# Optimization experiments

Hardware: AMD Instinct MI355X
Metric: run time of the kernel (lower is better)

The kernel has to match this reference:

```python
import jax, jax.numpy as jnp
import numpy as np

B, Hh, Ww, C = 8, 64, 64, 384
Dg = C // 2          # 192, per-group d_model
Di = Dg              # expand=1 -> d_inner = d_model
K = 2                # scan directions per group
S = 1                # d_state
R = -(-Dg // 16)     # dt_rank = ceil(d_model/16) = 12
Cout = 384


def setup_inputs() -> dict:
    key = jax.random.key(0)
    ks = jax.random.split(key, 30)
    n = lambda k, shp, s=0.05: (jax.random.normal(k, shp, jnp.float32) * s)
    inp = {
        "x": jax.random.normal(ks[0], (B, Hh * Ww, C), jnp.float32),
        "norm_g": jnp.ones((C,), jnp.float32),
        "norm_b": jnp.zeros((C,), jnp.float32),
        # DynamicChannelSorter (reduction=2)
        "r_w1": n(ks[1], (C // 2, C)), "r_b1": n(ks[2], (C // 2,)),
        "r_w2": n(ks[3], (C, C // 2)), "r_b2": n(ks[4], (C,)),
        # SS2D params stacked over 2 groups
        "in_proj_w": n(ks[5], (2, 2 * Di, Dg)),
        "conv_w": n(ks[6], (2, Di, 1, 3, 3), 0.1),
        "conv_b": n(ks[7], (2, Di), 0.02),
        "x_proj_w": n(ks[8], (2, K, R + 2 * S, Di)),
        "dt_proj_w": n(ks[9], (2, K, Di, R), 0.1),
        "dt_proj_b": n(ks[10], (2, K, Di), 0.5) - 3.0,   # softplus-inv of small dt
        "A_log": n(ks[11], (2, K, Di, S), 0.1),
        "Ds": jnp.ones((2, K, Di), jnp.float32),
        "out_norm_g": jnp.ones((2, Di), jnp.float32),
        "out_norm_b": jnp.zeros((2, Di), jnp.float32),
        "out_proj_w": n(ks[12], (2, Dg, Di)),
        # channel_interaction (reduction=16)
        "ci_w1": n(ks[13], (C // 16, C)), "ci_b1": n(ks[14], (C // 16,)),
        "ci_w2": n(ks[15], (C, C // 16)), "ci_b2": n(ks[16], (C,)),
        "proj_w": n(ks[17], (Cout, C)), "proj_b": n(ks[18], (Cout,)),
        "skip_scale": jnp.ones((1,), jnp.float32),
        "H": Hh, "W": Ww,
    }
    return inp


def _ln(x, g, b, eps=1e-5):
    m = x.mean(-1, keepdims=True)
    v = jnp.mean((x - m) ** 2, -1, keepdims=True)
    return (x - m) * jax.lax.rsqrt(v + eps) * g + b


def _selective_scan(xs, dts, Bm, Cm, A, D):
    # xs,dts: (B,K,Di,L); Bm,Cm: (B,K,S,L); A: (K,Di,S); D: (K,Di)
    dA = jnp.exp(dts[..., None] * A[None, :, :, None, :])              # (B,K,Di,L,S)
    dBx = dts[..., None] * jnp.swapaxes(Bm, -1, -2)[:, :, None] * xs[..., None]
    dA_t = jnp.moveaxis(dA, 3, 0)                                      # (L,B,K,Di,S)
    dBx_t = jnp.moveaxis(dBx, 3, 0)
    C_t = jnp.moveaxis(Cm, -1, 0)                                      # (L,B,K,S)
    h0 = jnp.zeros(dA.shape[:3] + (dA.shape[-1],), xs.dtype)           # (B,K,Di,S)

    def step(h, inp):
        a, bx, c = inp
        h = a * h + bx
        return h, jnp.einsum('bkcs,bks->bkc', h, c)

    _, ys = jax.lax.scan(step, h0, (dA_t, dBx_t, C_t))                 # (L,B,K,Di)
    ys = jnp.moveaxis(ys, 0, -1)                                       # (B,K,Di,L)
    return ys + D[None, :, :, None] * xs


def _ss2d(x, in_w, cw, cb, xp_w, dt_w, dt_b, A_log, D, on_g, on_b, op_w, vertical):
    # x: (B,H,W,Dg). VMamba-style SS2D with K=2 directions.
    b, h, w, _ = x.shape
    L = h * w
    xz = jnp.einsum('bhwc,dc->bhwd', x, in_w)                          # (B,H,W,2*Di)
    xc, z = jnp.split(xz, 2, axis=-1)
    xc = jnp.transpose(xc, (0, 3, 1, 2))                               # (B,Di,H,W)
    xc = jax.lax.conv_general_dilated(
        xc, cw, (1, 1), 'SAME', feature_group_count=Di,
        dimension_numbers=('NCHW', 'OIHW', 'NCHW')) + cb[None, :, None, None]
    xc = jax.nn.silu(xc)
    xf = jnp.transpose(xc, (0, 1, 3, 2)) if vertical else xc
    xflat = xf.reshape(b, Di, L)
    xs = jnp.stack([xflat, jnp.flip(xflat, -1)], axis=1)               # (B,K,Di,L)
    x_dbl = jnp.einsum('bkcl,kdc->bkdl', xs, xp_w)
    r = dt_w.shape[-1]
    dts, Bm, Cm = x_dbl[:, :, :r], x_dbl[:, :, r:r + S], x_dbl[:, :, r + S:r + 2 * S]
    dts = jax.nn.softplus(jnp.einsum('bkrl,kdr->bkdl', dts, dt_w) + dt_b[None, :, :, None])
    A = -jnp.exp(A_log)
    ys = _selective_scan(xs, dts, Bm, Cm, A, D)                        # (B,K,Di,L)
    y = ys[:, 0] + jnp.flip(ys[:, 1], -1)                              # cross-merge
    if vertical:
        y = jnp.transpose(y.reshape(b, Di, w, h), (0, 1, 3, 2))
    else:
        y = y.reshape(b, Di, h, w)
    y = jnp.transpose(y, (0, 2, 3, 1))                                 # (B,H,W,Di)
    y = _ln(y, on_g, on_b)
    y = y * jax.nn.silu(z)
    return jnp.einsum('bhwd,od->bhwo', y, op_w)


def reference(x, norm_g, norm_b, r_w1, r_b1, r_w2, r_b2, in_proj_w, conv_w,
              conv_b, x_proj_w, dt_proj_w, dt_proj_b, A_log, Ds, out_norm_g,
              out_norm_b, out_proj_w, ci_w1, ci_b1, ci_w2, ci_b2, proj_w,
              proj_b, skip_scale, H, W):
    b, n, c = x.shape
    residual = x
    xn = _ln(x, norm_g, norm_b)
    # dynamic channel sorter
    pool = xn.mean(axis=1)                                             # (B,C)
    scores = jax.nn.sigmoid(jax.nn.relu(pool @ r_w1.T + r_b1) @ r_w2.T + r_b2)
    sort_idx = jnp.argsort(-scores, axis=1)
    inv_idx = jnp.argsort(sort_idx, axis=1)
    x_sorted = jnp.take_along_axis(xn, sort_idx[:, None, :], axis=2)
    xsp = x_sorted.reshape(b, H, W, c)
    x1, x2 = jnp.split(xsp, 2, axis=-1)
    y1 = _ss2d(x1, in_proj_w[0], conv_w[0], conv_b[0], x_proj_w[0], dt_proj_w[0],
               dt_proj_b[0], A_log[0], Ds[0], out_norm_g[0], out_norm_b[0],
               out_proj_w[0], vertical=False)
    y2 = _ss2d(x2, in_proj_w[1], conv_w[1], conv_b[1], x_proj_w[1], dt_proj_w[1],
               dt_proj_b[1], A_log[1], Ds[1], out_norm_g[1], out_norm_b[1],
               out_proj_w[1], vertical=True)
    y_cat = jnp.concatenate([y1, y2], axis=-1).reshape(b, n, c)
    y_restored = jnp.take_along_axis(y_cat, inv_idx[:, None, :], axis=2)
    gate = jax.nn.sigmoid(jax.nn.relu(xn @ ci_w1.T + ci_b1) @ ci_w2.T + ci_b2)
    y_final = (y_restored * gate) @ proj_w.T + proj_b
    return residual + y_final * skip_scale
```

## Files before the change

### kernel.cpp

```cpp
#include <hip/hip_runtime.h>
#include <math.h>

#define NB 8
#define LTOK 4096
#define CH 384
#define DH 192
#define HH 64
#define WW 64
#define NCHK 128
#define CHS 32

static constexpr long BLC  = (long)NB * LTOK * CH;
static constexpr long CST  = (long)32 * NCHK * DH;

typedef unsigned short u16;
typedef u16   u16x8 __attribute__((ext_vector_type(8)));
typedef short s16x8 __attribute__((ext_vector_type(8)));
typedef float f32x4 __attribute__((ext_vector_type(4)));

__device__ inline u16 f2bf(float f){
  unsigned int u = __float_as_uint(f);
  return (u16)((u + 0x7FFFu + ((u >> 16) & 1u)) >> 16);
}
__device__ inline float bf2f(u16 h){ return __uint_as_float(((unsigned int)h) << 16); }
__device__ inline float fsigmoid(float x){ return 1.f / (1.f + __expf(-x)); }

#define SCOL(ml, c) ((c) ^ ((((ml) >> 2) & 3) << 4))

template<int NW>
__device__ inline float blockSum(float v, float* sm){
  #pragma unroll
  for (int o = 32; o > 0; o >>= 1) v += __shfl_down(v, o);
  int lane = threadIdx.x & 63, wv = threadIdx.x >> 6;
  if (lane == 0) sm[wv] = v;
  __syncthreads();
  if (threadIdx.x == 0){ float t = 0.f; for (int i = 0; i < NW; i++) t += sm[i]; sm[0] = t; }
  __syncthreads();
  float t = sm[0];
  __syncthreads();
  return t;
}

__global__ __launch_bounds__(128) void k_ln(const float* __restrict__ x,
    const float* __restrict__ g, const float* __restrict__ b, float* __restrict__ xn){
  __shared__ float sm[2];
  long row = blockIdx.x;
  int t = threadIdx.x;
  const float* xr = x + row * CH;
  float v0 = xr[t], v1 = xr[t + 128], v2 = xr[t + 256];
  float s = blockSum<2>(v0 + v1 + v2, sm);
  float m = s * (1.f / CH);
  float d0 = v0 - m, d1 = v1 - m, d2 = v2 - m;
  float vs = blockSum<2>(d0*d0 + d1*d1 + d2*d2, sm);
  float inv = rsqrtf(vs * (1.f / CH) + 1e-5f);
  float* o = xn + row * CH;
  o[t]       = d0 * inv * g[t]       + b[t];
  o[t + 128] = d1 * inv * g[t + 128] + b[t + 128];
  o[t + 256] = d2 * inv * g[t + 256] + b[t + 256];
}

__global__ __launch_bounds__(128) void k_pool(const float* __restrict__ xn, float* __restrict__ pp){
  int c = blockIdx.x * 128 + threadIdx.x;
  int chunk = blockIdx.y, b = blockIdx.z;
  long base = ((long)b * LTOK + chunk * 256) * CH;
  float s = 0.f;
  for (int n = 0; n < 256; n++) s += xn[base + (long)n * CH + c];
  pp[((long)b * 16 + chunk) * CH + c] = s;
}

__global__ __launch_bounds__(384) void k_score(const float* __restrict__ pp,
    const float* __restrict__ w1, const float* __restrict__ b1,
    const float* __restrict__ w2, const float* __restrict__ b2,
    int* __restrict__ sidx, int* __restrict__ inv){
  __shared__ float poolv[CH];
  __shared__ float hid[192];
  __shared__ float sc[CH];
  int b = blockIdx.x, t = threadIdx.x;
  float s = 0.f;
  for (int ch = 0; ch < 16; ch++) s += pp[((long)b * 16 + ch) * CH + t];
  poolv[t] = s * (1.f / LTOK);
  __syncthreads();
  if (t < 192){
    float h = b1[t];
    for (int c = 0; c < CH; c++) h += poolv[c] * w1[t * CH + c];
    hid[t] = fmaxf(h, 0.f);
  }
  __syncthreads();
  {
    float h = b2[t];
    for (int j = 0; j < 192; j++) h += hid[j] * w2[t * 192 + j];
    sc[t] = 1.f / (1.f + expf(-h));
  }
  __syncthreads();
  float mys = sc[t];
  int rank = 0;
  for (int j = 0; j < CH; j++){
    float o = sc[j];
    rank += (o > mys) || (o == mys && j < t);
  }
  sidx[b * CH + rank] = t;
  inv[b * CH + t] = rank;
}

__global__ __launch_bounds__(256) void k_cast(const float* __restrict__ s,
    u16* __restrict__ d, int n){
  int i = blockIdx.x * 256 + threadIdx.x;
  if (i < n) d[i] = f2bf(s[i]);
}

__global__ __launch_bounds__(256) void k_prepA(const float* __restrict__ alog,
    float* __restrict__ Atab){
  int i = blockIdx.x * 256 + threadIdx.x;
  if (i < 4 * 192) Atab[i] = -expf(alog[i]);
}

__global__ __launch_bounds__(256) void k_prepcw(const float* __restrict__ cw,
    u16* __restrict__ cwb){
  int i = blockIdx.x * 256 + threadIdx.x;
  if (i < 2 * 9 * DH){
    int g = i / (9 * DH); int r = i - g * 9 * DH;
    int tap = r / DH; int di = r - tap * DH;
    cwb[i] = f2bf(cw[((long)g * DH + di) * 9 + tap]);
  }
}

__global__ __launch_bounds__(384) void k_castgather(const float* __restrict__ xn,
    const int* __restrict__ sidx, u16* __restrict__ As){
  long row = blockIdx.x;
  int b = (int)(row >> 12);
  int t = threadIdx.x;
  int c = sidx[b * CH + t];
  As[row * CH + t] = f2bf(xn[row * CH + c]);
}

__global__ __launch_bounds__(256) void k_prepw(const float* __restrict__ w1,
    const float* __restrict__ b1, const float* __restrict__ w2,
    const int* __restrict__ sidx, u16* __restrict__ w1g, u16* __restrict__ w2p,
    float* __restrict__ b1p){
  int b = blockIdx.x, tid = threadIdx.x;
  if (b < NB){
    const int* sx = sidx + b * CH;
    for (int i = tid; i < 32 * CH; i += 256){
      int j = i / CH, r = i - j * CH;
      float v = (j < 24) ? w1[j * CH + sx[r]] : 0.f;
      w1g[(long)b * 32 * CH + i] = f2bf(v);
    }
  } else {
    for (int i = tid; i < CH * 32; i += 256){
      int n = i >> 5, j = i & 31;
      w2p[i] = f2bf((j < 24) ? w2[n * 24 + j] : 0.f);
    }
    if (tid < 32) b1p[tid] = (tid < 24) ? b1[tid] : 0.f;
  }
}

__global__ __launch_bounds__(256) void k_prepM(const float* __restrict__ dtw,
    const float* __restrict__ xpw, u16* __restrict__ Mw){
  int gk = blockIdx.y;
  int g = gk >> 1, k = gk & 1;
  int idx = blockIdx.x * 256 + threadIdx.x;
  int di = idx / 192, c = idx - di * 192;
  float s = 0.f;
  #pragma unroll
  for (int r = 0; r < 12; r++)
    s += dtw[((long)gk * 192 + di) * 12 + r] * xpw[(long)g * 5376 + (k * 14 + r) * 192 + c];
  Mw[(long)gk * 36864 + idx] = f2bf(s);
}

__global__ __launch_bounds__(256) void k_hid(const u16* __restrict__ As,
    const u16* __restrict__ w1g, const float* __restrict__ b1p,
    u16* __restrict__ hidp){
  __shared__ u16 sA[128 * 32];
  __shared__ u16 sB[32 * 32];
  int b = blockIdx.y;
  const u16* Ab = As + (long)b * LTOK * CH;
  const u16* Bb = w1g + (long)b * 32 * CH;
  int tid = threadIdx.x;
  int m0 = blockIdx.x * 128;
  int wv = tid >> 6, l = tid & 63;
  int wm = wv * 32;
  int kg = l >> 4, lr = l & 15;

  f32x4 acc[2][2];
  #pragma unroll
  for (int i = 0; i < 2; i++)
    #pragma unroll
    for (int j = 0; j < 2; j++)
      #pragma unroll
      for (int r = 0; r < 4; r++) acc[i][j][r] = 0.f;

  int aoffU[2], boffU[2];
  #pragma unroll
  for (int i = 0; i < 2; i++){
    int r = wm + i * 16 + lr;
    aoffU[i] = r * 32 + ((kg * 8) ^ ((r & 3) << 3));
  }
  #pragma unroll
  for (int j = 0; j < 2; j++){
    int r = j * 16 + lr;
    boffU[j] = r * 32 + ((kg * 8) ^ ((r & 3) << 3));
  }

  u16x8 ra[2], rbv;
  #pragma unroll
  for (int q = 0; q < 2; q++){
    int i = q * 256 + tid; int row = i >> 2, sl = i & 3, ss = sl ^ (row & 3);
    ra[q] = *(const u16x8*)(Ab + (long)(m0 + row) * CH + ss * 8);
  }
  if (tid < 128){
    int row = tid >> 2, sl = tid & 3, ss = sl ^ (row & 3);
    rbv = *(const u16x8*)(Bb + (long)row * CH + ss * 8);
  }

  const int nks = CH / 32;
  for (int ks = 0; ks < nks; ks++){
    __syncthreads();
    #pragma unroll
    for (int q = 0; q < 2; q++){
      int i = q * 256 + tid; int row = i >> 2, sl = i & 3;
      *(u16x8*)(sA + row * 32 + sl * 8) = ra[q];
    }
    if (tid < 128){
      int row = tid >> 2, sl = tid & 3;
      *(u16x8*)(sB + row * 32 + sl * 8) = rbv;
    }
    __syncthreads();
    if (ks + 1 < nks){
      int k0 = (ks + 1) * 32;
      #pragma unroll
      for (int q = 0; q < 2; q++){
        int i = q * 256 + tid; int row = i >> 2, sl = i & 3, ss = sl ^ (row & 3);
        ra[q] = *(const u16x8*)(Ab + (long)(m0 + row) * CH + k0 + ss * 8);
      }
      if (tid < 128){
        int row = tid >> 2, sl = tid & 3, ss = sl ^ (row & 3);
        rbv = *(const u16x8*)(Bb + (long)row * CH + k0 + ss * 8);
      }
    }
    s16x8 af[2], bfr[2];
    #pragma unroll
    for (int i = 0; i < 2; i++) af[i] = *(const s16x8*)(sA + aoffU[i]);
    #pragma unroll
    for (int j = 0; j < 2; j++) bfr[j] = *(const s16x8*)(sB + boffU[j]);
    #pragma unroll
    for (int i = 0; i < 2; i++)
      #pragma unroll
      for (int j = 0; j < 2; j++)
        acc[i][j] = __builtin_amdgcn_mfma_f32_16x16x32_bf16(af[i], bfr[j], acc[i][j], 0, 0, 0);
  }

  #pragma unroll
  for (int i = 0; i < 2; i++)
    #pragma unroll
    for (int j = 0; j < 2; j++)
      #pragma unroll
      for (int r = 0; r < 4; r++){
        int m = m0 + wm + i * 16 + kg * 4 + r;
        int n = j * 16 + lr;
        float v = fmaxf(acc[i][j][r] + b1p[n], 0.f);
        hidp[((long)b * LTOK + m) * 32 + n] = f2bf(v);
      }
}

template<int BN, int MODE>
__global__ __launch_bounds__(256) void k_mm(
    const u16* __restrict__ A, int lda, long aOuter, long aInner,
    const u16* __restrict__ B, long bInner,
    float* __restrict__ Cf, u16* __restrict__ Ch,
    long cOuter, long cInner, int ldc,
    int K, int innerCnt,
    const float* __restrict__ bias, const float* __restrict__ resid,
    const float* __restrict__ skip,
    const u16* __restrict__ gy, const int* __restrict__ ginv){
  constexpr int BM = 128;
  constexpr int AI = 2;
  constexpr int BI = (BN * 32) / (256 * 8);
  constexpr int NJ = BN / 32;
  __shared__ u16 sA[BM * 32];
  __shared__ u16 sB[BN * 32];

  int bz = blockIdx.z;
  int bo = bz / innerCnt, bi_ = bz - bo * innerCnt;
  const u16* Ab = A + (long)bo * aOuter + (long)bi_ * aInner;
  const u16* Bb = B + (long)bi_ * bInner;
  int tid = threadIdx.x;
  int m0 = blockIdx.y * BM, n0 = blockIdx.x * BN;
  int wv = tid >> 6, l = tid & 63;
  int wm = (wv >> 1) * 64, wn = (wv & 1) * (BN / 2);
  int kg = l >> 4, lr = l & 15;

  f32x4 acc[4][NJ];
  #pragma unroll
  for (int i = 0; i < 4; i++)
    #pragma unroll
    for (int j = 0; j < NJ; j++)
      #pragma unroll
      for (int r = 0; r < 4; r++) acc[i][j][r] = 0.f;

  int aoffU[4], boffU[NJ];
  #pragma unroll
  for (int i = 0; i < 4; i++){
    int r = wm + i * 16 + lr;
    aoffU[i] = r * 32 + ((kg * 8) ^ ((r & 3) << 3));
  }
  #pragma unroll
  for (int j = 0; j < NJ; j++){
    int r = wn + j * 16 + lr;
    boffU[j] = r * 32 + ((kg * 8) ^ ((r & 3) << 3));
  }

  u16x8 ra[AI], rb[BI];
  #pragma unroll
  for (int q = 0; q < AI; q++){
    int i = q * 256 + tid; int row = i >> 2, sl = i & 3, ss = sl ^ (row & 3);
    ra[q] = *(const u16x8*)(Ab + (long)(m0 + row) * lda + ss * 8);
  }
  #pragma unroll
  for (int q = 0; q < BI; q++){
    int i = q * 256 + tid; int row = i >> 2, sl = i & 3, ss = sl ^ (row & 3);
    rb[q] = *(const u16x8*)(Bb + (long)(n0 + row) * K + ss * 8);
  }

  int nks = K >> 5;
  for (int ks = 0; ks < nks; ks++){
    __syncthreads();
    #pragma unroll
    for (int q = 0; q < AI; q++){
      int i = q * 256 + tid; int row = i >> 2, sl = i & 3;
      *(u16x8*)(sA + row * 32 + sl * 8) = ra[q];
    }
    #pragma unroll
    for (int q = 0; q < BI; q++){
      int i = q * 256 + tid; int row = i >> 2, sl = i & 3;
      *(u16x8*)(sB + row * 32 + sl * 8) = rb[q];
    }
    __syncthreads();
    if (ks + 1 < nks){
      int k0 = (ks + 1) * 32;
      #pragma unroll
      for (int q = 0; q < AI; q++){
        int i = q * 256 + tid; int row = i >> 2, sl = i & 3, ss = sl ^ (row & 3);
        ra[q] = *(const u16x8*)(Ab + (long)(m0 + row) * lda + k0 + ss * 8);
      }
      #pragma unroll
      for (int q = 0; q < BI; q++){
        int i = q * 256 + tid; int row = i >> 2, sl = i & 3, ss = sl ^ (row & 3);
        rb[q] = *(const u16x8*)(Bb + (long)(n0 + row) * K + k0 + ss * 8);
      }
    }
    s16x8 af[4];
    #pragma unroll
    for (int i = 0; i < 4; i++) af[i] = *(const s16x8*)(sA + aoffU[i]);
    s16x8 bfr[NJ];
    #pragma unroll
    for (int j = 0; j < NJ; j++) bfr[j] = *(const s16x8*)(sB + boffU[j]);
    #pragma unroll
    for (int i = 0; i < 4; i++)
      #pragma unroll
      for (int j = 0; j < NJ; j++)
        acc[i][j] = __builtin_amdgcn_mfma_f32_16x16x32_bf16(af[i], bfr[j], acc[i][j], 0, 0, 0);
  }

  long zc = (long)bo * cOuter + (long)bi_ * cInner;
  #pragma unroll
  for (int i = 0; i < 4; i++){
    #pragma unroll
    for (int j = 0; j < NJ; j++){
      #pragma unroll
      for (int r = 0; r < 4; r++){
        int m = m0 + wm + i * 16 + kg * 4 + r;
        int n = n0 + wn + j * 16 + lr;
        float v = acc[i][j][r];
        if constexpr (MODE == 1){
          if (n < 192) ((u16*)Cf)[zc + (long)m * 192 + n] = f2bf(v);
          else         Ch[zc + (long)m * 192 + (n - 192)] = f2bf(v);
        } else if constexpr (MODE == 2){
          Ch[zc + (long)m * ldc + n] = f2bf(v);
        } else if constexpr (MODE == 3){
          float vb = v + bias[n];
          long o = (long)m * ldc + n;
          Cf[o] = resid[o] + skip[0] * vb;
        } else {
          float gate = fsigmoid(v + bias[n]);
          int bt = m >> 12;
          float yr = bf2f(gy[(long)m * ldc + ginv[bt * CH + n]]);
          Ch[(long)m * ldc + n] = f2bf(yr * gate);
        }
      }
    }
  }
}

__global__ __launch_bounds__(256) void k_dt(
    const u16* __restrict__ xcvh, const u16* __restrict__ Mw,
    const float* __restrict__ dtb, const float* __restrict__ Atab,
    const float* __restrict__ bc, u16* __restrict__ pk16,
    float* __restrict__ cP, float* __restrict__ cS){
  constexpr int BM = 128, AI = 2, NJ = 2;
  __shared__ unsigned sMem[BM * 64];
  u16* sA = (u16*)sMem;
  u16* sB = (u16*)(sMem + 2048);

  int z = blockIdx.z;
  int bg = z >> 1, kk_ = z & 1, g = bg & 1, gk = g * 2 + kk_;
  const u16* Ab = xcvh + (long)bg * LTOK * 192;
  const u16* Bb = Mw + (long)gk * 36864;
  int tid = threadIdx.x;
  int m0 = blockIdx.y * BM, n0 = blockIdx.x * 64;
  int wv = tid >> 6, l = tid & 63;
  int wm = (wv >> 1) * 64, wn = (wv & 1) * 32;
  int kg = l >> 4, lr = l & 15;

  f32x4 acc[4][NJ];
  #pragma unroll
  for (int i = 0; i < 4; i++)
    #pragma unroll
    for (int j = 0; j < NJ; j++)
      #pragma unroll
      for (int r = 0; r < 4; r++) acc[i][j][r] = 0.f;

  int aoffU[4], boffU[NJ];
  #pragma unroll
  for (int i = 0; i < 4; i++){
    int r = wm + i * 16 + lr;
    aoffU[i] = r * 32 + ((kg * 8) ^ ((r & 3) << 3));
  }
  #pragma unroll
  for (int j = 0; j < NJ; j++){
    int r = wn + j * 16 + lr;
    boffU[j] = r * 32 + ((kg * 8) ^ ((r & 3) << 3));
  }

  u16x8 ra[AI], rb0;
  #pragma unroll
  for (int q = 0; q < AI; q++){
    int i = q * 256 + tid; int row = i >> 2, sl = i & 3, ss = sl ^ (row & 3);
    ra[q] = *(const u16x8*)(Ab + (long)(m0 + row) * 192 + ss * 8);
  }
  {
    int row = tid >> 2, sl = tid & 3, ss = sl ^ (row & 3);
    rb0 = *(const u16x8*)(Bb + (long)(n0 + row) * 192 + ss * 8);
  }

  const int nks = 6;
  for (int ks = 0; ks < nks; ks++){
    __syncthreads();
    #pragma unroll
    for (int q = 0; q < AI; q++){
      int i = q * 256 + tid; int row = i >> 2, sl = i & 3;
      *(u16x8*)(sA + row * 32 + sl * 8) = ra[q];
    }
    {
      int row = tid >> 2, sl = tid & 3;
      *(u16x8*)(sB + row * 32 + sl * 8) = rb0;
    }
    __syncthreads();
    if (ks + 1 < nks){
      int k0 = (ks + 1) * 32;
      #pragma unroll
      for (int q = 0; q < AI; q++){
        int i = q * 256 + tid; int row = i >> 2, sl = i & 3, ss = sl ^ (row & 3);
        ra[q] = *(const u16x8*)(Ab + (long)(m0 + row) * 192 + k0 + ss * 8);
      }
      {
        int row = tid >> 2, sl = tid & 3, ss = sl ^ (row & 3);
        rb0 = *(const u16x8*)(Bb + (long)(n0 + row) * 192 + k0 + ss * 8);
      }
    }
    s16x8 af[4], bfr[NJ];
    #pragma unroll
    for (int i = 0; i < 4; i++) af[i] = *(const s16x8*)(sA + aoffU[i]);
    #pragma unroll
    for (int j = 0; j < NJ; j++) bfr[j] = *(const s16x8*)(sB + boffU[j]);
    #pragma unroll
    for (int i = 0; i < 4; i++)
      #pragma unroll
      for (int j = 0; j < NJ; j++)
        acc[i][j] = __builtin_amdgcn_mfma_f32_16x16x32_bf16(af[i], bfr[j], acc[i][j], 0, 0, 0);
  }

  unsigned pkreg[4][NJ][4];
  #pragma unroll
  for (int i = 0; i < 4; i++){
    #pragma unroll
    for (int j = 0; j < NJ; j++){
      #pragma unroll
      for (int r = 0; r < 4; r++){
        int m = m0 + wm + i * 16 + kg * 4 + r;
        int n = n0 + wn + j * 16 + lr;
        float rr = acc[i][j][r] + dtb[gk * 192 + n];
        float dtv = __logf(1.f + __expf(rr));
        float av  = __expf(Atab[gk * 192 + n] * dtv);
        float Bv  = bc[((long)z * LTOK + m) * 2];
        float xv  = bf2f(xcvh[((long)bg * LTOK + m) * 192 + n]);
        pk16[((long)z * LTOK + m) * 192 + n] = f2bf(dtv);
        pkreg[i][j][r] = ((unsigned)f2bf(dtv * Bv * xv) << 16) | (unsigned)f2bf(av);
      }
    }
  }

  __syncthreads();
  #pragma unroll
  for (int i = 0; i < 4; i++){
    #pragma unroll
    for (int j = 0; j < NJ; j++){
      #pragma unroll
      for (int r = 0; r < 4; r++){
        int ml = wm + i * 16 + kg * 4 + r;
        int cl = wn + j * 16 + lr;
        sMem[ml * 64 + SCOL(ml, cl)] = pkreg[i][j][r];
      }
    }
  }
  __syncthreads();

  int cc = tid >> 6, nn = tid & 63;
  float P = 1.f, S = 0.f;
  if (kk_ == 0){
    for (int s = 0; s < CHS; s++){
      int row = cc * CHS + s;
      unsigned v = sMem[row * 64 + SCOL(row, nn)];
      float a = bf2f((u16)(v & 0xFFFFu));
      float dBx = bf2f((u16)(v >> 16));
      P *= a; S = a * S + dBx;
    }
  } else {
    for (int s = CHS - 1; s >= 0; s--){
      int row = cc * CHS + s;
      unsigned v = sMem[row * 64 + SCOL(row, nn)];
      float a = bf2f((u16)(v & 0xFFFFu));
      float dBx = bf2f((u16)(v >> 16));
      P *= a; S = a * S + dBx;
    }
  }
  int cglob = (kk_ == 0) ? (blockIdx.y * 4 + cc)
                         : ((LTOK - m0) / CHS - cc - 1);
  long idx = ((long)z * NCHK + cglob) * 192 + n0 + nn;
  cP[idx] = P;
  cS[idx] = S;
}

__global__ __launch_bounds__(192) void k_conv(const u16* __restrict__ xch,
    const u16* __restrict__ cwb, const float* __restrict__ cb,
    const float* __restrict__ xpw, u16* __restrict__ xcvh,
    float* __restrict__ bc){
  __shared__ float red[8][4][25];
  int tid = threadIdx.x;
  int chg = tid % 24, pp = tid / 24;
  int p = blockIdx.x * 8 + pp;
  int bg = blockIdx.y; int g = bg & 1;
  int h = p >> 6, w = p & 63;
  int di = chg * 8;
  long sb = (long)bg * LTOK;

  u16x8 wv[9];
  #pragma unroll
  for (int t = 0; t < 9; t++)
    wv[t] = *(const u16x8*)(cwb + ((long)g * 9 + t) * DH + di);

  float acc[8];
  #pragma unroll
  for (int j = 0; j < 8; j++) acc[j] = cb[g * DH + di + j];

  #pragma unroll
  for (int dh = -1; dh <= 1; dh++){
    int hh = h + dh; if (hh < 0 || hh >= HH) continue;
    #pragma unroll
    for (int dw = -1; dw <= 1; dw++){
      int ww2 = w + dw; if (ww2 < 0 || ww2 >= WW) continue;
      u16x8 xv = *(const u16x8*)(xch + (sb + hh * WW + ww2) * DH + di);
      int t = (dh + 1) * 3 + (dw + 1);
      #pragma unroll
      for (int j = 0; j < 8; j++) acc[j] += bf2f(wv[t][j]) * bf2f(xv[j]);
    }
  }

  u16x8 ov;
  #pragma unroll
  for (int j = 0; j < 8; j++){
    float s = acc[j];
    acc[j] = s * fsigmoid(s);
    ov[j] = f2bf(acc[j]);
  }
  int lscan = (g == 0) ? p : (w * HH + h);
  *(u16x8*)(xcvh + (sb + lscan) * DH + di) = ov;

  #pragma unroll
  for (int j = 0; j < 4; j++){
    int k = j >> 1, ci = j & 1;
    const float* wl = xpw + (long)g * 5376 + (k * 14 + 12 + ci) * 192 + di;
    float sacc = 0.f;
    #pragma unroll
    for (int q = 0; q < 8; q++) sacc += acc[q] * wl[q];
    red[pp][j][chg] = sacc;
  }
  __syncthreads();
  if (tid < 32){
    int pos = tid >> 2, j = tid & 3;
    float ssum = 0.f;
    #pragma unroll
    for (int q = 0; q < 24; q++) ssum += red[pos][j][q];
    int p2 = blockIdx.x * 8 + pos;
    int h2 = p2 >> 6, w2 = p2 & 63;
    int ls = (g == 0) ? p2 : (w2 * HH + h2);
    int k = j >> 1;
    bc[(((long)(bg * 2 + k)) * LTOK + ls) * 2 + (j & 1)] = ssum;
  }
}

__global__ __launch_bounds__(192) void k_scan_p2(const float* __restrict__ cP,
    const float* __restrict__ cS, float* __restrict__ h0){
  int z = blockIdx.x;
  int di = threadIdx.x;
  float h = 0.f;
  for (int c = 0; c < NCHK; c++){
    long idx = ((long)z * NCHK + c) * 192 + di;
    h0[idx] = h;
    h = cP[idx] * h + cS[idx];
  }
}

__global__ __launch_bounds__(192) void k_scan_p3(const u16* __restrict__ pk16,
    const u16* __restrict__ xcvh, const float* __restrict__ bc,
    const float* __restrict__ Atab, const float* __restrict__ ds,
    const float* __restrict__ h0, u16* __restrict__ ydir){
  int bg = blockIdx.x, c = blockIdx.y;
  int g = bg & 1;
  int di = threadIdx.x;
  const u16* xc = xcvh + (long)bg * LTOK * 192 + di;
  u16* yo = ydir + (long)bg * LTOK * 192 + di;
  #pragma unroll
  for (int k = 0; k < 2; k++){
    int z = bg * 2 + k, gk = g * 2 + k;
    float Dv = ds[gk * 192 + di];
    float Av = Atab[gk * 192 + di];
    const u16* pk = pk16 + (long)z * LTOK * 192 + di;
    const float* bcp = bc + (long)z * LTOK * 2;
    int cc = (k == 0) ? c : (NCHK - 1 - c);
    float h = h0[((long)z * NCHK + cc) * 192 + di];
    int l  = (k == 0) ? c * CHS : (c * CHS + CHS - 1);
    int dl = (k == 0) ? 1 : -1;
    for (int s = 0; s < CHS; s++, l += dl){
      float dtv = bf2f(pk[(long)l * 192]);
      float av  = __expf(Av * dtv);
      float xv  = bf2f(xc[(long)l * 192]);
      float Bv  = bcp[l * 2], Cv = bcp[l * 2 + 1];
      h = av * h + dtv * Bv * xv;
      float y = h * Cv + Dv * xv;
      if (k == 0) yo[(long)l * 192] = f2bf(y);
      else        yo[(long)l * 192] = f2bf(bf2f(yo[(long)l * 192]) + y);
    }
  }
}

__global__ __launch_bounds__(192) void k_combine(const u16* __restrict__ ydir,
    const u16* __restrict__ zh, const float* __restrict__ ong, const float* __restrict__ onb,
    u16* __restrict__ yab){
  __shared__ float sm[3];
  int p = blockIdx.x; int bg = blockIdx.y; int g = bg & 1;
  int h = p >> 6, w = p & 63;
  int l = (g == 0) ? p : (w * HH + h);
  int di = threadIdx.x;
  float y = bf2f(ydir[((long)bg * LTOK + l) * DH + di]);
  float s = blockSum<3>(y, sm);
  float m = s * (1.f / DH);
  float d = y - m;
  float vs = blockSum<3>(d * d, sm);
  float inv = rsqrtf(vs * (1.f / DH) + 1e-5f);
  float yl = d * inv * ong[g * DH + di] + onb[g * DH + di];
  float z = bf2f(zh[((long)bg * LTOK + p) * DH + di]);
  yab[((long)bg * LTOK + p) * DH + di] = f2bf(yl * z * fsigmoid(z));
}

extern "C" void kernel_launch(void* const* d_in, const int* in_sizes, int n_in,
                              void* d_out, int out_size, void* d_ws, size_t ws_size,
                              hipStream_t stream){
  const float* x       = (const float*)d_in[0];
  const float* norm_g  = (const float*)d_in[1];
  const float* norm_b  = (const float*)d_in[2];
  const float* r_w1    = (const float*)d_in[3];
  const float* r_b1    = (const float*)d_in[4];
  const float* r_w2    = (const float*)d_in[5];
  const float* r_b2    = (const float*)d_in[6];
  const float* in_proj = (const float*)d_in[7];
  const float* conv_w  = (const float*)d_in[8];
  const float* conv_b  = (const float*)d_in[9];
  const float* xp_w    = (const float*)d_in[10];
  const float* dt_w    = (const float*)d_in[11];
  const float* dt_b    = (const float*)d_in[12];
  const float* A_log   = (const float*)d_in[13];
  const float* Ds      = (const float*)d_in[14];
  const float* on_g    = (const float*)d_in[15];
  const float* on_b    = (const float*)d_in[16];
  const float* op_w    = (const float*)d_in[17];
  const float* ci_w1   = (const float*)d_in[18];
  const float* ci_b1   = (const float*)d_in[19];
  const float* ci_w2   = (const float*)d_in[20];
  const float* ci_b2   = (const float*)d_in[21];
  const float* proj_w  = (const float*)d_in[22];
  const float* proj_b  = (const float*)d_in[23];
  const float* skip    = (const float*)d_in[24];
  float* out = (float*)d_out;
  float* ws  = (float*)d_ws;

  float* xn   = ws;
  float* xcb  = ws + BLC;
  float* R3   = ws + 2 * BLC;
  float* R4   = R3 + BLC / 2;
  float* R5   = R4 + BLC / 2;
  float* pp   = R5 + BLC / 2;
  int*  sidx  = (int*)(pp + NB * 16 * CH);
  int*  inv   = sidx + NB * CH;
  u16*  wip   = (u16*)(inv + NB * CH);
  u16*  wop   = wip + 2 * 384 * 192;
  u16*  wpj   = wop + 2 * 192 * 192;
  u16*  w1g   = wpj + 384 * 384;
  u16*  w2p   = w1g + NB * 32 * CH;
  u16*  Mw    = w2p + CH * 32;
  u16*  cwb   = Mw + 4 * 192 * 192;
  float* b1p  = (float*)(cwb + 2 * 9 * DH);
  float* Atab = b1p + 32;
  u16*  hidp  = (u16*)(Atab + 4 * 192);
  float* bc   = (float*)(hidp + (long)NB * LTOK * 32);
  float* cP   = bc + 32 * LTOK * 2;
  float* cS   = cP + CST;
  float* h0   = cS + CST;

  size_t need = ((size_t)(2 * BLC) + 3 * (BLC / 2) + NB * 16 * CH + 32 * LTOK * 2 + 3 * CST + 64) * 4
              + (size_t)(2 * NB * CH) * 4 + (size_t)(4 * 192 + 32) * 4
              + ((size_t)2*384*192 + 2*192*192 + 384*384 + NB*32*CH + CH*32 + 4*192*192
                 + 2*9*DH + (size_t)NB * LTOK * 32) * 2
              + 8192;
  if (ws_size < need) return;

  u16*  As   = (u16*)R5;
  u16*  zh   = (u16*)R3;
  u16*  xcbh = (u16*)xcb;
  u16*  xcvh = (u16*)R4;
  u16*  pk16 = (u16*)ws;
  u16*  ydir = (u16*)R5;
  u16*  yab  = (u16*)R4;
  u16*  ycat = (u16*)R3;
  u16*  gab  = (u16*)xcb;

  k_ln<<<NB * LTOK, 128, 0, stream>>>(x, norm_g, norm_b, xn);
  k_cast<<<(2*384*192 + 255)/256, 256, 0, stream>>>(in_proj, wip, 2*384*192);
  k_cast<<<(2*192*192 + 255)/256, 256, 0, stream>>>(op_w,    wop, 2*192*192);
  k_cast<<<(384*384   + 255)/256, 256, 0, stream>>>(proj_w,  wpj, 384*384);
  k_prepA<<<3, 256, 0, stream>>>(A_log, Atab);
  k_prepcw<<<(2*9*DH + 255)/256, 256, 0, stream>>>(conv_w, cwb);
  k_prepM<<<dim3(144, 4), 256, 0, stream>>>(dt_w, xp_w, Mw);
  k_pool<<<dim3(3, 16, NB), 128, 0, stream>>>(xn, pp);
  k_score<<<NB, 384, 0, stream>>>(pp, r_w1, r_b1, r_w2, r_b2, sidx, inv);
  k_castgather<<<NB * LTOK, 384, 0, stream>>>(xn, sidx, As);
  k_prepw<<<NB + 1, 256, 0, stream>>>(ci_w1, ci_b1, ci_w2, sidx, w1g, w2p, b1p);

  k_mm<128, 1><<<dim3(3, 32, 16), 256, 0, stream>>>(
      As, CH, (long)LTOK * CH, 192,
      wip, (long)384 * 192,
      (float*)xcbh, zh, (long)2 * LTOK * DH, (long)LTOK * DH, 0,
      192, 2, nullptr, nullptr, nullptr, nullptr, nullptr);

  k_hid<<<dim3(32, NB), 256, 0, stream>>>(As, w1g, b1p, hidp);

  k_conv<<<dim3(LTOK / 8, NB * 2), 192, 0, stream>>>(xcbh, cwb, conv_b, xp_w, xcvh, bc);

  k_dt<<<dim3(3, 32, 32), 256, 0, stream>>>(xcvh, Mw, dt_b, Atab, bc, pk16, cP, cS);

  k_scan_p2<<<32, 192, 0, stream>>>(cP, cS, h0);
  k_scan_p3<<<dim3(NB * 2, NCHK), 192, 0, stream>>>(pk16, xcvh, bc, Atab, Ds, h0, ydir);

  k_combine<<<dim3(LTOK, NB * 2), 192, 0, stream>>>(ydir, zh, on_g, on_b, yab);

  k_mm<64, 2><<<dim3(3, 32, 16), 256, 0, stream>>>(
      yab, DH, (long)2 * LTOK * DH, (long)LTOK * DH,
      wop, (long)192 * 192,
      nullptr, ycat, (long)LTOK * CH, 192, CH,
      192, 2, nullptr, nullptr, nullptr, nullptr, nullptr);

  k_mm<128, 4><<<dim3(3, 256, 1), 256, 0, stream>>>(
      hidp, 32, 0, 0,
      w2p, 0,
      nullptr, gab, 0, 0, CH,
      32, 1, ci_b2, nullptr, nullptr, ycat, inv);

  k_mm<128, 3><<<dim3(3, 256, 1), 256, 0, stream>>>(
      gab, CH, 0, 0,
      wpj, 0,
      out, nullptr, 0, 0, CH,
      CH, 1, proj_b, x, skip, nullptr, nullptr);
}
```

Baseline: 395.2 us.

## Fuse combine LayerNorm and gating into scan pass, stage x tile in LDS

The scan pass now keeps both directions' chunk outputs in registers and sums them there, instead of writing one direction to memory and read-modify-writing it for the other. It then performs the out_norm LayerNorm and z·silu(z) gating in-block through shared memory, which removes the separate combine kernel and the ydir intermediate round trip. In k_dt, the x tile is staged into shared memory with vector loads and the per-column bias and A values are hoisted, replacing scattered 2-byte global loads in the epilogue. The cost is higher register and LDS use in the scan kernel, plus a one-pass variance formula that is less numerically stable.

```diff
diff --git a/kernel.cpp b/kernel.cpp
--- a/kernel.cpp
+++ b/kernel.cpp
@@ -398,8 +398,9 @@
     float* __restrict__ cP, float* __restrict__ cS){
   constexpr int BM = 128, AI = 2, NJ = 2;
   __shared__ unsigned sMem[BM * 64];
-  u16* sA = (u16*)sMem;
-  u16* sB = (u16*)(sMem + 2048);
+  u16* sA  = (u16*)sMem;
+  u16* sB  = (u16*)(sMem + 2048);
+  u16* xvT = (u16*)(sMem + 3072);
 
   int z = blockIdx.z;
   int bg = z >> 1, kk_ = z & 1, g = bg & 1, gk = g * 2 + kk_;
@@ -411,6 +412,14 @@
   int wm = (wv >> 1) * 64, wn = (wv & 1) * 32;
   int kg = l >> 4, lr = l & 15;
 
+  #pragma unroll
+  for (int q = 0; q < 4; q++){
+    int i8 = q * 256 + tid;
+    int row = i8 >> 3, c8 = i8 & 7;
+    u16x8 v = *(const u16x8*)(Ab + (long)(m0 + row) * 192 + n0 + c8 * 8);
+    *(u16x8*)(xvT + row * 72 + c8 * 8) = v;
+  }
+
   f32x4 acc[4][NJ];
   #pragma unroll
   for (int i = 0; i < 4; i++)
@@ -480,19 +489,27 @@
   }
 
   unsigned pkreg[4][NJ][4];
+  float dtbj[NJ], Atlj[NJ];
+  #pragma unroll
+  for (int j = 0; j < NJ; j++){
+    int n = n0 + wn + j * 16 + lr;
+    dtbj[j] = dtb[gk * 192 + n];
+    Atlj[j] = Atab[gk * 192 + n];
+  }
   #pragma unroll
   for (int i = 0; i < 4; i++){
     #pragma unroll
-    for (int j = 0; j < NJ; j++){
-      #pragma unroll
-      for (int r = 0; r < 4; r++){
-        int m = m0 + wm + i * 16 + kg * 4 + r;
+    for (int r = 0; r < 4; r++){
+      int ml = wm + i * 16 + kg * 4 + r;
+      int m = m0 + ml;
+      float Bv = bc[((long)z * LTOK + m) * 2];
+      #pragma unroll
+      for (int j = 0; j < NJ; j++){
         int n = n0 + wn + j * 16 + lr;
-        float rr = acc[i][j][r] + dtb[gk * 192 + n];
+        float rr = acc[i][j][r] + dtbj[j];
         float dtv = __logf(1.f + __expf(rr));
-        float av  = __expf(Atab[gk * 192 + n] * dtv);
-        float Bv  = bc[((long)z * LTOK + m) * 2];
-        float xv  = bf2f(xcvh[((long)bg * LTOK + m) * 192 + n]);
+        float av  = __expf(Atlj[j] * dtv);
+        float xv  = bf2f(xvT[ml * 72 + wn + j * 16 + lr]);
         pk16[((long)z * LTOK + m) * 192 + n] = f2bf(dtv);
         pkreg[i][j][r] = ((unsigned)f2bf(dtv * Bv * xv) << 16) | (unsigned)f2bf(av);
       }
@@ -623,53 +640,92 @@
 __global__ __launch_bounds__(192) void k_scan_p3(const u16* __restrict__ pk16,
     const u16* __restrict__ xcvh, const float* __restrict__ bc,
     const float* __restrict__ Atab, const float* __restrict__ ds,
-    const float* __restrict__ h0, u16* __restrict__ ydir){
+    const float* __restrict__ h0, const u16* __restrict__ zh,
+    const float* __restrict__ ong, const float* __restrict__ onb,
+    u16* __restrict__ yab){
+  __shared__ float yl[CHS][193];
+  __shared__ float red[2][32][6];
+  __shared__ float minv[2][32];
   int bg = blockIdx.x, c = blockIdx.y;
   int g = bg & 1;
   int di = threadIdx.x;
   const u16* xc = xcvh + (long)bg * LTOK * 192 + di;
-  u16* yo = ydir + (long)bg * LTOK * 192 + di;
-  #pragma unroll
-  for (int k = 0; k < 2; k++){
-    int z = bg * 2 + k, gk = g * 2 + k;
-    float Dv = ds[gk * 192 + di];
-    float Av = Atab[gk * 192 + di];
+  int l0 = c * CHS;
+  float yv[CHS];
+
+  {
+    int z = bg * 2, gk = g * 2;
+    float Dv = ds[gk * 192 + di], Av = Atab[gk * 192 + di];
     const u16* pk = pk16 + (long)z * LTOK * 192 + di;
     const float* bcp = bc + (long)z * LTOK * 2;
-    int cc = (k == 0) ? c : (NCHK - 1 - c);
-    float h = h0[((long)z * NCHK + cc) * 192 + di];
-    int l  = (k == 0) ? c * CHS : (c * CHS + CHS - 1);
-    int dl = (k == 0) ? 1 : -1;
-    for (int s = 0; s < CHS; s++, l += dl){
+    float h = h0[((long)z * NCHK + c) * 192 + di];
+    #pragma unroll
+    for (int s = 0; s < CHS; s++){
+      int l = l0 + s;
       float dtv = bf2f(pk[(long)l * 192]);
       float av  = __expf(Av * dtv);
       float xv  = bf2f(xc[(long)l * 192]);
       float Bv  = bcp[l * 2], Cv = bcp[l * 2 + 1];
       h = av * h + dtv * Bv * xv;
-      float y = h * Cv + Dv * xv;
-      if (k == 0) yo[(long)l * 192] = f2bf(y);
-      else        yo[(long)l * 192] = f2bf(bf2f(yo[(long)l * 192]) + y);
-    }
-  }
-}
-
-__global__ __launch_bounds__(192) void k_combine(const u16* __restrict__ ydir,
-    const u16* __restrict__ zh, const float* __restrict__ ong, const float* __restrict__ onb,
-    u16* __restrict__ yab){
-  __shared__ float sm[3];
-  int p = blockIdx.x; int bg = blockIdx.y; int g = bg & 1;
-  int h = p >> 6, w = p & 63;
-  int l = (g == 0) ? p : (w * HH + h);
-  int di = threadIdx.x;
-  float y = bf2f(ydir[((long)bg * LTOK + l) * DH + di]);
-  float s = blockSum<3>(y, sm);
-  float m = s * (1.f / DH);
-  float d = y - m;
-  float vs = blockSum<3>(d * d, sm);
-  float inv = rsqrtf(vs * (1.f / DH) + 1e-5f);
-  float yl = d * inv * ong[g * DH + di] + onb[g * DH + di];
-  float z = bf2f(zh[((long)bg * LTOK + p) * DH + di]);
-  yab[((long)bg * LTOK + p) * DH + di] = f2bf(yl * z * fsigmoid(z));
+      yv[s] = h * Cv + Dv * xv;
+    }
+  }
+  {
+    int z = bg * 2 + 1, gk = g * 2 + 1;
+    float Dv = ds[gk * 192 + di], Av = Atab[gk * 192 + di];
+    const u16* pk = pk16 + (long)z * LTOK * 192 + di;
+    const float* bcp = bc + (long)z * LTOK * 2;
+    int cc = NCHK - 1 - c;
+    float h = h0[((long)z * NCHK + cc) * 192 + di];
+    #pragma unroll
+    for (int s = CHS - 1; s >= 0; s--){
+      int l = l0 + s;
+      float dtv = bf2f(pk[(long)l * 192]);
+      float av  = __expf(Av * dtv);
+      float xv  = bf2f(xc[(long)l * 192]);
+      float Bv  = bcp[l * 2], Cv = bcp[l * 2 + 1];
+      h = av * h + dtv * Bv * xv;
+      yv[s] += h * Cv + Dv * xv;
+    }
+  }
+
+  #pragma unroll
+  for (int s = 0; s < CHS; s++) yl[s][di] = yv[s];
+  __syncthreads();
+  {
+    int pos = di & 31, seg = di >> 5;
+    float s1 = 0.f, s2 = 0.f;
+    #pragma unroll
+    for (int q = 0; q < 32; q++){
+      float v = yl[pos][seg * 32 + q];
+      s1 += v; s2 += v * v;
+    }
+    red[0][pos][seg] = s1;
+    red[1][pos][seg] = s2;
+  }
+  __syncthreads();
+  if (di < 32){
+    float s1 = 0.f, s2 = 0.f;
+    #pragma unroll
+    for (int q = 0; q < 6; q++){ s1 += red[0][di][q]; s2 += red[1][di][q]; }
+    float m = s1 * (1.f / DH);
+    float var = s2 * (1.f / DH) - m * m;
+    minv[0][di] = m;
+    minv[1][di] = rsqrtf(var + 1e-5f);
+  }
+  __syncthreads();
+
+  float gng = ong[g * 192 + di], gnb = onb[g * 192 + di];
+  long zbase = (long)bg * LTOK;
+  #pragma unroll
+  for (int s = 0; s < CHS; s++){
+    int l = l0 + s;
+    int p = (g == 0) ? l : ((l & 63) * 64 + (l >> 6));
+    float m = minv[0][s], inv = minv[1][s];
+    float yln = (yv[s] - m) * inv * gng + gnb;
+    float z = bf2f(zh[(zbase + p) * 192 + di]);
+    yab[(zbase + p) * 192 + di] = f2bf(yln * z * fsigmoid(z));
+  }
 }
 
 extern "C" void kernel_launch(void* const* d_in, const int* in_sizes, int n_in,
@@ -738,8 +794,7 @@
   u16*  xcbh = (u16*)xcb;
   u16*  xcvh = (u16*)R4;
   u16*  pk16 = (u16*)ws;
-  u16*  ydir = (u16*)R5;
-  u16*  yab  = (u16*)R4;
+  u16*  yab  = (u16*)R5;
   u16*  ycat = (u16*)R3;
   u16*  gab  = (u16*)xcb;
 
@@ -768,9 +823,9 @@
   k_dt<<<dim3(3, 32, 32), 256, 0, stream>>>(xcvh, Mw, dt_b, Atab, bc, pk16, cP, cS);
 
   k_scan_p2<<<32, 192, 0, stream>>>(cP, cS, h0);
-  k_scan_p3<<<dim3(NB * 2, NCHK), 192, 0, stream>>>(pk16, xcvh, bc, Atab, Ds, h0, ydir);
-
-  k_combine<<<dim3(LTOK, NB * 2), 192, 0, stream>>>(ydir, zh, on_g, on_b, yab);
+
+  k_scan_p3<<<dim3(NB * 2, NCHK), 192, 0, stream>>>(
+      pk16, xcvh, bc, Atab, Ds, h0, zh, on_g, on_b, yab);
 
   k_mm<64, 2><<<dim3(3, 32, 16), 256, 0, stream>>>(
       yab, DH, (long)2 * LTOK * DH, (long)LTOK * DH,
```

Result: faster. 369.8 us (-6.4%).
